# Performance work log

Hardware: AMD Instinct MI355X
Metric: run time of the kernel (lower is better)

Reference implementation:

```python
import jax, jax.numpy as jnp
import numpy as np

D_MODEL = 1024
NUM_HEADS = 16
HEAD_DIM = D_MODEL // NUM_HEADS  # 64
# NOTE: the original module passes scale=attention_head_size, so scores are
# MULTIPLIED by head_dim (64), not divided by sqrt(head_dim). Faithful quirk.
SCALE = float(HEAD_DIM)


def setup_inputs() -> dict:
    key = jax.random.key(0)
    ks = jax.random.split(key, 6)
    bs, s, d = 2, 2048, D_MODEL
    q = jax.random.normal(ks[0], (bs, s, d), dtype=jnp.float32)
    k = jax.random.normal(ks[1], (bs, s, d), dtype=jnp.float32)
    v = jax.random.normal(ks[2], (bs, s, d), dtype=jnp.float32)
    # nn.Linear weights, shape (out, in); no bias (qkv_bias=False)
    init = 1.0 / np.sqrt(d)
    Wq = jax.random.uniform(ks[3], (d, d), jnp.float32, -init, init)
    Wk = jax.random.uniform(ks[4], (d, d), jnp.float32, -init, init)
    Wv = jax.random.uniform(ks[5], (d, d), jnp.float32, -init, init)
    return {"q": q, "k": k, "v": v, "Wq": Wq, "Wk": Wk, "Wv": Wv}


def _split_heads(x):
    bs, s, _ = x.shape
    return x.reshape(bs, s, NUM_HEADS, HEAD_DIM).transpose(0, 2, 1, 3)  # bhsd


def reference(q, k, v, Wq, Wk, Wv):
    bs, s, d = q.shape
    qh = _split_heads(q @ Wq.T)  # [b,h,s,hd]
    kh = _split_heads(k @ Wk.T)
    vh = _split_heads(v @ Wv.T)
    sims = jnp.einsum('bhqd,bhkd->bhqk', qh, kh) * SCALE
    attn = jax.nn.softmax(sims, axis=-1)
    out = jnp.einsum('bhqk,bhkd->bhqd', attn, vh)  # [b,h,s,hd]
    out = out.transpose(0, 2, 1, 3).reshape(bs, s, d)
    return out
```

## Files before the change

kernel.cpp:

```cpp
#include <hip/hip_runtime.h>


typedef _Float16 half4 __attribute__((ext_vector_type(4)));
typedef _Float16 half8 __attribute__((ext_vector_type(8)));
typedef float floatx4 __attribute__((ext_vector_type(4)));

#define MFMA_F16(a, b, c) __builtin_amdgcn_mfma_f32_16x16x32_f16((a), (b), (c), 0, 0, 0)

constexpr int SEQ = 2048;
constexpr int DM = 1024;
constexpr int NH = 16;
constexpr int HD = 64;
constexpr float QSCALE = 92.33248261689366f;

__device__ inline void split4(const float4 f, half4& h, half4& l) {
  h[0] = (_Float16)f.x; l[0] = (_Float16)(f.x - (float)h[0]);
  h[1] = (_Float16)f.y; l[1] = (_Float16)(f.y - (float)h[1]);
  h[2] = (_Float16)f.z; l[2] = (_Float16)(f.z - (float)h[2]);
  h[3] = (_Float16)f.w; l[3] = (_Float16)(f.w - (float)h[3]);
}

__global__ __launch_bounds__(256) void convert_kernel(
    const float* __restrict__ x, const float* __restrict__ W,
    _Float16* __restrict__ xh, _Float16* __restrict__ xl,
    _Float16* __restrict__ Wh, _Float16* __restrict__ Wl, int do_lo)
{
  if (blockIdx.x < 4096) {
    int idx = blockIdx.x * 256 + threadIdx.x;
    float4 f = ((const float4*)x)[idx];
    half4 h, l; split4(f, h, l);
    *(half4*)(xh + (size_t)idx * 4) = h;
    if (do_lo) *(half4*)(xl + (size_t)idx * 4) = l;
  } else {
    int idx = (blockIdx.x - 4096) * 256 + threadIdx.x;
    float4 f = ((const float4*)W)[idx];
    half4 h, l; split4(f, h, l);
    *(half4*)(Wh + (size_t)idx * 4) = h;
    if (do_lo) *(half4*)(Wl + (size_t)idx * 4) = l;
  }
}

__global__ __launch_bounds__(256, 1) void proj_kernel(
    const _Float16* __restrict__ Ahg, const _Float16* __restrict__ Alg,
    const _Float16* __restrict__ Bhg, const _Float16* __restrict__ Blg,
    _Float16* __restrict__ yh, _Float16* __restrict__ yl,
    float scale, int three)
{
  __shared__ __align__(16) _Float16 Ahs[128][72];
  __shared__ __align__(16) _Float16 Als[128][72];
  __shared__ __align__(16) _Float16 Bhs[128][72];
  __shared__ __align__(16) _Float16 Bls[128][72];

  const int tid = threadIdx.x;
  const int bm = blockIdx.x;
  const int bn = blockIdx.y;
  const int lane = tid & 63, l15 = lane & 15, quad = lane >> 4;
  const int w = tid >> 6, wm = w >> 1, wn = w & 1;

  int row_[4], col_[4];
  #pragma unroll
  for (int i = 0; i < 4; i++) { int c = i * 256 + tid; row_[i] = c >> 3; col_[i] = (c & 7) * 8; }

  half8 pah[4], pal[4], pbh[4], pbl[4];
  #pragma unroll
  for (int i = 0; i < 4; i++) {
    pah[i] = *(const half8*)(Ahg + (size_t)(bm * 128 + row_[i]) * DM + col_[i]);
    pbh[i] = *(const half8*)(Bhg + (size_t)(bn * 128 + row_[i]) * DM + col_[i]);
    if (three) {
      pal[i] = *(const half8*)(Alg + (size_t)(bm * 128 + row_[i]) * DM + col_[i]);
      pbl[i] = *(const half8*)(Blg + (size_t)(bn * 128 + row_[i]) * DM + col_[i]);
    }
  }

  floatx4 acc[4][4];
  #pragma unroll
  for (int mt = 0; mt < 4; mt++)
    #pragma unroll
    for (int nt = 0; nt < 4; nt++)
      acc[mt][nt] = (floatx4){0.f, 0.f, 0.f, 0.f};

  for (int kk = 0; kk < DM; kk += 64) {
    __syncthreads();
    #pragma unroll
    for (int i = 0; i < 4; i++) {
      *(half8*)&Ahs[row_[i]][col_[i]] = pah[i];
      *(half8*)&Bhs[row_[i]][col_[i]] = pbh[i];
      if (three) {
        *(half8*)&Als[row_[i]][col_[i]] = pal[i];
        *(half8*)&Bls[row_[i]][col_[i]] = pbl[i];
      }
    }
    if (kk + 64 < DM) {
      #pragma unroll
      for (int i = 0; i < 4; i++) {
        pah[i] = *(const half8*)(Ahg + (size_t)(bm * 128 + row_[i]) * DM + kk + 64 + col_[i]);
        pbh[i] = *(const half8*)(Bhg + (size_t)(bn * 128 + row_[i]) * DM + kk + 64 + col_[i]);
        if (three) {
          pal[i] = *(const half8*)(Alg + (size_t)(bm * 128 + row_[i]) * DM + kk + 64 + col_[i]);
          pbl[i] = *(const half8*)(Blg + (size_t)(bn * 128 + row_[i]) * DM + kk + 64 + col_[i]);
        }
      }
    }
    __syncthreads();

    #pragma unroll
    for (int kc = 0; kc < 2; kc++) {
      half8 ah[4], bh_[4], al[4], bl[4];
      #pragma unroll
      for (int t = 0; t < 4; t++) {
        ah[t]  = *(const half8*)&Ahs[wm * 64 + t * 16 + l15][kc * 32 + quad * 8];
        bh_[t] = *(const half8*)&Bhs[wn * 64 + t * 16 + l15][kc * 32 + quad * 8];
        if (three) {
          al[t] = *(const half8*)&Als[wm * 64 + t * 16 + l15][kc * 32 + quad * 8];
          bl[t] = *(const half8*)&Bls[wn * 64 + t * 16 + l15][kc * 32 + quad * 8];
        }
      }
      if (three) {
        #pragma unroll
        for (int mt = 0; mt < 4; mt++)
          #pragma unroll
          for (int nt = 0; nt < 4; nt++) {
            floatx4 t0 = MFMA_F16(ah[mt], bh_[nt], acc[mt][nt]);
            t0 = MFMA_F16(ah[mt], bl[nt], t0);
            acc[mt][nt] = MFMA_F16(al[mt], bh_[nt], t0);
          }
      } else {
        #pragma unroll
        for (int mt = 0; mt < 4; mt++)
          #pragma unroll
          for (int nt = 0; nt < 4; nt++)
            acc[mt][nt] = MFMA_F16(ah[mt], bh_[nt], acc[mt][nt]);
      }
    }
  }

  #pragma unroll
  for (int mt = 0; mt < 4; mt++)
    #pragma unroll
    for (int nt = 0; nt < 4; nt++)
      #pragma unroll
      for (int r = 0; r < 4; r++) {
        int gm = bm * 128 + wm * 64 + mt * 16 + quad * 4 + r;
        int gn = bn * 128 + wn * 64 + nt * 16 + l15;
        int b = gm >> 11, s = gm & 2047;
        int h = gn >> 6, d = gn & 63;
        size_t idx = ((size_t)(b * NH + h) * SEQ + s) * HD + d;
        float val = acc[mt][nt][r] * scale;
        _Float16 hi = (_Float16)val;
        yh[idx] = hi;
        if (three) yl[idx] = (_Float16)(val - (float)hi);
      }
}

__global__ __launch_bounds__(256) void transpose_v(const _Float16* __restrict__ vh,
                                                   _Float16* __restrict__ vhT)
{
  __shared__ __align__(16) _Float16 T[128][72];
  const int bh = blockIdx.x, sc = blockIdx.y, tid = threadIdx.x;
  const _Float16* src = vh + ((size_t)bh * SEQ + sc * 128) * HD;
  #pragma unroll
  for (int i = 0; i < 4; i++) {
    int c = i * 256 + tid, row = c >> 3, off = (c & 7) * 8;
    *(half8*)&T[row][off] = *(const half8*)(src + (size_t)row * HD + off);
  }
  __syncthreads();
  _Float16* dst = vhT + (size_t)bh * HD * SEQ + sc * 128;
  #pragma unroll
  for (int i = 0; i < 4; i++) {
    int c = i * 256 + tid, hd = c >> 4, off = (c & 15) * 8;
    int base32 = off & ~31, qsel = (off >> 3) & 3;
    half8 vv;
    #pragma unroll
    for (int j = 0; j < 8; j++) {
      int s_local = base32 + 16 * (j >> 2) + 4 * qsel + (j & 3);
      vv[j] = T[s_local][hd];
    }
    *(half8*)(dst + (size_t)hd * SEQ + off) = vv;
  }
}

__global__ __launch_bounds__(256, 4) void flash_kernel(
    const _Float16* __restrict__ qh_hi, const _Float16* __restrict__ qh_lo,
    const _Float16* __restrict__ kh_hi, const _Float16* __restrict__ kh_lo,
    const _Float16* __restrict__ vhT, float* __restrict__ Op, float2* __restrict__ ml)
{
  __shared__ __align__(16) _Float16 Kh[64][72];
  __shared__ __align__(16) _Float16 Kl[64][72];
  __shared__ __align__(16) _Float16 Vt[64][72];

  const int bh = blockIdx.x;
  const int qb = blockIdx.y;
  const int kh = blockIdx.z;
  const int tid = threadIdx.x;
  const int wq = tid >> 6;
  const int lane = tid & 63, l15 = lane & 15, quad = lane >> 4;

  const size_t bh_off = (size_t)bh * SEQ * HD;
  const _Float16* __restrict__ kh_p = kh_hi + bh_off;
  const _Float16* __restrict__ kl_p = kh_lo + bh_off;
  const _Float16* __restrict__ vt_p = vhT + (size_t)bh * HD * SEQ;
  const int qrow0 = qb * 128 + wq * 32;

  half8 bqh[2][2], bql[2][2];
  #pragma unroll
  for (int g = 0; g < 2; g++) {
    const _Float16* qp_h = qh_hi + bh_off + (size_t)(qrow0 + g * 16 + l15) * HD;
    const _Float16* qp_l = qh_lo + bh_off + (size_t)(qrow0 + g * 16 + l15) * HD;
    #pragma unroll
    for (int kc = 0; kc < 2; kc++) {
      bqh[g][kc] = *(const half8*)(qp_h + kc * 32 + quad * 8);
      bql[g][kc] = *(const half8*)(qp_l + kc * 32 + quad * 8);
    }
  }

  const int c0 = tid, c1 = tid + 256;
  const int row0 = c0 >> 3, off0 = (c0 & 7) * 8;
  const int row1 = c1 >> 3, off1 = (c1 & 7) * 8;

  float m_[2] = {-3.0e38f, -3.0e38f};
  float l_[2] = {0.f, 0.f};
  floatx4 Oacc[2][4];
  #pragma unroll
  for (int g = 0; g < 2; g++)
    #pragma unroll
    for (int nd = 0; nd < 4; nd++) Oacc[g][nd] = (floatx4){0.f, 0.f, 0.f, 0.f};

  const int kt0 = kh * 16;
  for (int kt = kt0; kt < kt0 + 16; kt++) {
    const int kbase = kt * 64;
    __syncthreads();
    {
      half8 t0 = *(const half8*)(kh_p + (size_t)(kbase + row0) * HD + off0);
      half8 t1 = *(const half8*)(kh_p + (size_t)(kbase + row1) * HD + off1);
      half8 t2 = *(const half8*)(kl_p + (size_t)(kbase + row0) * HD + off0);
      half8 t3 = *(const half8*)(kl_p + (size_t)(kbase + row1) * HD + off1);
      half8 t4 = *(const half8*)(vt_p + (size_t)row0 * SEQ + kbase + off0);
      half8 t5 = *(const half8*)(vt_p + (size_t)row1 * SEQ + kbase + off1);
      *(half8*)&Kh[row0][off0] = t0;
      *(half8*)&Kh[row1][off1] = t1;
      *(half8*)&Kl[row0][off0] = t2;
      *(half8*)&Kl[row1][off1] = t3;
      *(half8*)&Vt[row0][off0] = t4;
      *(half8*)&Vt[row1][off1] = t5;
    }
    __syncthreads();

    floatx4 sacc[2][4];
    #pragma unroll
    for (int nt = 0; nt < 4; nt++) {
      half8 akh0 = *(const half8*)&Kh[nt * 16 + l15][quad * 8];
      half8 akh1 = *(const half8*)&Kh[nt * 16 + l15][32 + quad * 8];
      half8 akl0 = *(const half8*)&Kl[nt * 16 + l15][quad * 8];
      half8 akl1 = *(const half8*)&Kl[nt * 16 + l15][32 + quad * 8];
      #pragma unroll
      for (int g = 0; g < 2; g++) {
        floatx4 s4 = (floatx4){0.f, 0.f, 0.f, 0.f};
        s4 = MFMA_F16(akh0, bqh[g][0], s4);
        s4 = MFMA_F16(akh1, bqh[g][1], s4);
        s4 = MFMA_F16(akh0, bql[g][0], s4);
        s4 = MFMA_F16(akh1, bql[g][1], s4);
        s4 = MFMA_F16(akl0, bqh[g][0], s4);
        s4 = MFMA_F16(akl1, bqh[g][1], s4);
        sacc[g][nt] = s4;
      }
    }

    #pragma unroll
    for (int g = 0; g < 2; g++) {
      float rmax = sacc[g][0][0];
      #pragma unroll
      for (int nt = 0; nt < 4; nt++)
        #pragma unroll
        for (int r = 0; r < 4; r++) rmax = fmaxf(rmax, sacc[g][nt][r]);
      rmax = fmaxf(rmax, __shfl_xor(rmax, 16, 64));
      rmax = fmaxf(rmax, __shfl_xor(rmax, 32, 64));
      const float mnew = fmaxf(m_[g], rmax);
      const float alpha = exp2f(m_[g] - mnew);
      m_[g] = mnew;

      float rsum = 0.f;
      #pragma unroll
      for (int nt = 0; nt < 4; nt++)
        #pragma unroll
        for (int r = 0; r < 4; r++) {
          float p = exp2f(sacc[g][nt][r] - mnew);
          sacc[g][nt][r] = p;
          rsum += p;
        }
      rsum += __shfl_xor(rsum, 16, 64);
      rsum += __shfl_xor(rsum, 32, 64);
      l_[g] = l_[g] * alpha + rsum;

      half8 bp8[2];
      #pragma unroll
      for (int kc = 0; kc < 2; kc++)
        #pragma unroll
        for (int j = 0; j < 8; j++)
          bp8[kc][j] = (_Float16)sacc[g][2 * kc + (j >> 2)][j & 3];

      #pragma unroll
      for (int nd = 0; nd < 4; nd++) {
        half8 av0 = *(const half8*)&Vt[nd * 16 + l15][quad * 8];
        half8 av1 = *(const half8*)&Vt[nd * 16 + l15][32 + quad * 8];
        Oacc[g][nd][0] *= alpha; Oacc[g][nd][1] *= alpha;
        Oacc[g][nd][2] *= alpha; Oacc[g][nd][3] *= alpha;
        Oacc[g][nd] = MFMA_F16(av0, bp8[0], Oacc[g][nd]);
        Oacc[g][nd] = MFMA_F16(av1, bp8[1], Oacc[g][nd]);
      }
    }
  }

  const size_t fqbase = (size_t)bh * SEQ + qrow0;
  #pragma unroll
  for (int g = 0; g < 2; g++) {
    const size_t fq = fqbase + g * 16 + l15;
    float* ob = Op + ((size_t)kh * 65536 + fq) * HD;
    #pragma unroll
    for (int nd = 0; nd < 4; nd++) {
      float4 vv;
      vv.x = Oacc[g][nd][0]; vv.y = Oacc[g][nd][1];
      vv.z = Oacc[g][nd][2]; vv.w = Oacc[g][nd][3];
      *(float4*)(ob + nd * 16 + quad * 4) = vv;
    }
    if (quad == 0) ml[kh * 65536 + fq] = make_float2(m_[g], l_[g]);
  }
}

__global__ __launch_bounds__(256) void merge_kernel(const float* __restrict__ Op,
                                                    const float2* __restrict__ ml,
                                                    float* __restrict__ out)
{
  const int tid = threadIdx.x;
  const int fq = blockIdx.x * 64 + (tid >> 2);
  const int dp = (tid & 3) * 16;
  float2 m0 = ml[fq], m1 = ml[65536 + fq];
  float M = fmaxf(m0.x, m1.x);
  float w0 = exp2f(m0.x - M), w1 = exp2f(m1.x - M);
  float rinv = 1.0f / (m0.y * w0 + m1.y * w1);
  int bh = fq >> 11, s = fq & 2047, b = bh >> 4, h = bh & 15;
  float* ob = out + ((size_t)(b * SEQ + s)) * DM + h * HD + dp;
  const float* p0 = Op + (size_t)fq * HD + dp;
  const float* p1 = p0 + (size_t)65536 * HD;
  #pragma unroll
  for (int j = 0; j < 4; j++) {
    float4 a = *(const float4*)(p0 + 4 * j);
    float4 c = *(const float4*)(p1 + 4 * j);
    float4 r;
    r.x = (a.x * w0 + c.x * w1) * rinv;
    r.y = (a.y * w0 + c.y * w1) * rinv;
    r.z = (a.z * w0 + c.z * w1) * rinv;
    r.w = (a.w * w0 + c.w * w1) * rinv;
    *(float4*)(ob + 4 * j) = r;
  }
}

extern "C" void kernel_launch(void* const* d_in, const int* in_sizes, int n_in,
                              void* d_out, int out_size, void* d_ws, size_t ws_size,
                              hipStream_t stream) {
  const float* q  = (const float*)d_in[0];
  const float* k  = (const float*)d_in[1];
  const float* v  = (const float*)d_in[2];
  const float* Wq = (const float*)d_in[3];
  const float* Wk = (const float*)d_in[4];
  const float* Wv = (const float*)d_in[5];
  float* out = (float*)d_out;

  char* W = (char*)d_ws;
  const size_t MiB = 1ull << 20;
  _Float16* qh_hi = (_Float16*)(W + 0 * MiB);
  _Float16* qh_lo = (_Float16*)(W + 8 * MiB);
  _Float16* kh_hi = (_Float16*)(W + 16 * MiB);
  _Float16* kh_lo = (_Float16*)(W + 24 * MiB);
  _Float16* vhT   = (_Float16*)(W + 32 * MiB);
  _Float16* vh    = (_Float16*)(W + 40 * MiB);
  _Float16* xh    = (_Float16*)(W + 48 * MiB);
  _Float16* xl    = (_Float16*)(W + 56 * MiB);
  _Float16* Wh    = (_Float16*)(W + 64 * MiB);
  _Float16* Wl    = (_Float16*)(W + 66 * MiB);
  float*    Op    = (float*)  (W + 40 * MiB);
  float2*   mlp   = (float2*) (W + 72 * MiB);

  convert_kernel<<<5120, 256, 0, stream>>>(q, Wq, xh, xl, Wh, Wl, 1);
  proj_kernel<<<dim3(32, 8), 256, 0, stream>>>(xh, xl, Wh, Wl, qh_hi, qh_lo, QSCALE, 1);
  convert_kernel<<<5120, 256, 0, stream>>>(k, Wk, xh, xl, Wh, Wl, 1);
  proj_kernel<<<dim3(32, 8), 256, 0, stream>>>(xh, xl, Wh, Wl, kh_hi, kh_lo, 1.0f, 1);
  convert_kernel<<<5120, 256, 0, stream>>>(v, Wv, xh, xl, Wh, Wl, 0);
  proj_kernel<<<dim3(32, 8), 256, 0, stream>>>(xh, xl, Wh, Wl, vh, vh, 1.0f, 0);

  transpose_v<<<dim3(32, 16), 256, 0, stream>>>(vh, vhT);
  flash_kernel<<<dim3(32, 16, 2), 256, 0, stream>>>(qh_hi, qh_lo, kh_hi, kh_lo, vhT, Op, mlp);
  merge_kernel<<<1024, 256, 0, stream>>>(Op, mlp, out);
}
```

Baseline: 346.1 us.

## Fuse activation split into a batched QKV projection and swizzle LDS tiles

The separate per-projection convert kernels for activations are removed. The projection kernel now reads fp32 q/k/v directly and splits them into hi/lo halves while staging to LDS. The three projections run in a single launch using a z grid dimension, with weights pre-converted by one combined kernel, and launch bounds are raised to allow two blocks per CU. LDS padding is replaced by an XOR swizzle in both the projection and flash kernels, and flash block indices are remapped into a 1D grid. This cuts launches and intermediate global traffic and gives more parallel blocks. The cost is extra conversion ALU work inside the GEMM loop and higher register pressure.

```diff
diff --git a/kernel.cpp b/kernel.cpp
--- a/kernel.cpp
+++ b/kernel.cpp
@@ -20,36 +20,37 @@
   h[3] = (_Float16)f.w; l[3] = (_Float16)(f.w - (float)h[3]);
 }
 
-__global__ __launch_bounds__(256) void convert_kernel(
-    const float* __restrict__ x, const float* __restrict__ W,
-    _Float16* __restrict__ xh, _Float16* __restrict__ xl,
-    _Float16* __restrict__ Wh, _Float16* __restrict__ Wl, int do_lo)
+__global__ __launch_bounds__(256) void convert_w(
+    const float* __restrict__ Wq, const float* __restrict__ Wk,
+    const float* __restrict__ Wv, _Float16* __restrict__ Wbase)
 {
-  if (blockIdx.x < 4096) {
-    int idx = blockIdx.x * 256 + threadIdx.x;
-    float4 f = ((const float4*)x)[idx];
-    half4 h, l; split4(f, h, l);
-    *(half4*)(xh + (size_t)idx * 4) = h;
-    if (do_lo) *(half4*)(xl + (size_t)idx * 4) = l;
-  } else {
-    int idx = (blockIdx.x - 4096) * 256 + threadIdx.x;
-    float4 f = ((const float4*)W)[idx];
-    half4 h, l; split4(f, h, l);
-    *(half4*)(Wh + (size_t)idx * 4) = h;
-    if (do_lo) *(half4*)(Wl + (size_t)idx * 4) = l;
-  }
-}
-
-__global__ __launch_bounds__(256, 1) void proj_kernel(
-    const _Float16* __restrict__ Ahg, const _Float16* __restrict__ Alg,
-    const _Float16* __restrict__ Bhg, const _Float16* __restrict__ Blg,
-    _Float16* __restrict__ yh, _Float16* __restrict__ yl,
-    float scale, int three)
+  const int z = blockIdx.x >> 10;
+  const int idx = (blockIdx.x & 1023) * 256 + threadIdx.x;
+  const float* __restrict__ src = (z == 0) ? Wq : (z == 1) ? Wk : Wv;
+  float4 f = ((const float4*)src)[idx];
+  half4 h, l; split4(f, h, l);
+  _Float16* Wh = Wbase + (size_t)z * 2097152;
+  *(half4*)(Wh + (size_t)idx * 4) = h;
+  if (z < 2) *(half4*)(Wh + 1048576 + (size_t)idx * 4) = l;
+}
+
+__global__ __launch_bounds__(256, 2) void proj_kernel(
+    const float* __restrict__ q, const float* __restrict__ k, const float* __restrict__ v,
+    const _Float16* __restrict__ Wbase,
+    _Float16* __restrict__ qh_hi, _Float16* __restrict__ qh_lo,
+    _Float16* __restrict__ kh_hi, _Float16* __restrict__ kh_lo,
+    _Float16* __restrict__ vh)
 {
-  __shared__ __align__(16) _Float16 Ahs[128][72];
-  __shared__ __align__(16) _Float16 Als[128][72];
-  __shared__ __align__(16) _Float16 Bhs[128][72];
-  __shared__ __align__(16) _Float16 Bls[128][72];
+  __shared__ __align__(16) _Float16 Ahs[128][64];
+  __shared__ __align__(16) _Float16 Als[128][64];
+  __shared__ __align__(16) _Float16 Bhs[128][64];
+  __shared__ __align__(16) _Float16 Bls[128][64];
+
+  const int z = blockIdx.z;
+  const float* __restrict__ x = (z == 0) ? q : (z == 1) ? k : v;
+  const _Float16* __restrict__ Whg = Wbase + (size_t)z * 2097152;
+  const _Float16* __restrict__ Wlg = Whg + 1048576;
+  const int three = (z != 2);
 
   const int tid = threadIdx.x;
   const int bm = blockIdx.x;
@@ -57,19 +58,24 @@
   const int lane = tid & 63, l15 = lane & 15, quad = lane >> 4;
   const int w = tid >> 6, wm = w >> 1, wn = w & 1;
 
-  int row_[4], col_[4];
-  #pragma unroll
-  for (int i = 0; i < 4; i++) { int c = i * 256 + tid; row_[i] = c >> 3; col_[i] = (c & 7) * 8; }
-
-  half8 pah[4], pal[4], pbh[4], pbl[4];
+  int rowi[4], chi[4], swc[4];
   #pragma unroll
   for (int i = 0; i < 4; i++) {
-    pah[i] = *(const half8*)(Ahg + (size_t)(bm * 128 + row_[i]) * DM + col_[i]);
-    pbh[i] = *(const half8*)(Bhg + (size_t)(bn * 128 + row_[i]) * DM + col_[i]);
-    if (three) {
-      pal[i] = *(const half8*)(Alg + (size_t)(bm * 128 + row_[i]) * DM + col_[i]);
-      pbl[i] = *(const half8*)(Blg + (size_t)(bn * 128 + row_[i]) * DM + col_[i]);
-    }
+    int c = i * 256 + tid;
+    rowi[i] = c >> 3; chi[i] = c & 7;
+    swc[i] = (chi[i] ^ (rowi[i] & 7)) * 8;
+  }
+
+  float4 pa[4][2];
+  half8 pbh[4], pbl[4];
+  #pragma unroll
+  for (int i = 0; i < 4; i++) {
+    const float* ar = x + (size_t)(bm * 128 + rowi[i]) * DM + chi[i] * 8;
+    pa[i][0] = *(const float4*)ar;
+    pa[i][1] = *(const float4*)(ar + 4);
+    pbh[i] = *(const half8*)(Whg + (size_t)(bn * 128 + rowi[i]) * DM + chi[i] * 8);
+    if (three)
+      pbl[i] = *(const half8*)(Wlg + (size_t)(bn * 128 + rowi[i]) * DM + chi[i] * 8);
   }
 
   floatx4 acc[4][4];
@@ -83,36 +89,41 @@
     __syncthreads();
     #pragma unroll
     for (int i = 0; i < 4; i++) {
-      *(half8*)&Ahs[row_[i]][col_[i]] = pah[i];
-      *(half8*)&Bhs[row_[i]][col_[i]] = pbh[i];
-      if (three) {
-        *(half8*)&Als[row_[i]][col_[i]] = pal[i];
-        *(half8*)&Bls[row_[i]][col_[i]] = pbl[i];
-      }
+      half4 h0, l0, h1, l1;
+      split4(pa[i][0], h0, l0);
+      split4(pa[i][1], h1, l1);
+      half8 hh, ll;
+      #pragma unroll
+      for (int j = 0; j < 4; j++) { hh[j] = h0[j]; hh[j + 4] = h1[j]; ll[j] = l0[j]; ll[j + 4] = l1[j]; }
+      *(half8*)&Ahs[rowi[i]][swc[i]] = hh;
+      *(half8*)&Als[rowi[i]][swc[i]] = ll;
+      *(half8*)&Bhs[rowi[i]][swc[i]] = pbh[i];
+      if (three) *(half8*)&Bls[rowi[i]][swc[i]] = pbl[i];
     }
     if (kk + 64 < DM) {
       #pragma unroll
       for (int i = 0; i < 4; i++) {
-        pah[i] = *(const half8*)(Ahg + (size_t)(bm * 128 + row_[i]) * DM + kk + 64 + col_[i]);
-        pbh[i] = *(const half8*)(Bhg + (size_t)(bn * 128 + row_[i]) * DM + kk + 64 + col_[i]);
+        const float* ar = x + (size_t)(bm * 128 + rowi[i]) * DM + kk + 64 + chi[i] * 8;
+        pa[i][0] = *(const float4*)ar;
+        pa[i][1] = *(const float4*)(ar + 4);
+        pbh[i] = *(const half8*)(Whg + (size_t)(bn * 128 + rowi[i]) * DM + kk + 64 + chi[i] * 8);
+        if (three)
+          pbl[i] = *(const half8*)(Wlg + (size_t)(bn * 128 + rowi[i]) * DM + kk + 64 + chi[i] * 8);
+      }
+    }
+    __syncthreads();
+
+    #pragma unroll
+    for (int kc = 0; kc < 2; kc++) {
+      const int swz = ((kc * 4 + quad) ^ (l15 & 7)) * 8;
+      half8 ah[4], bh_[4], al[4], bl[4];
+      #pragma unroll
+      for (int t = 0; t < 4; t++) {
+        ah[t]  = *(const half8*)&Ahs[wm * 64 + t * 16 + l15][swz];
+        bh_[t] = *(const half8*)&Bhs[wn * 64 + t * 16 + l15][swz];
         if (three) {
-          pal[i] = *(const half8*)(Alg + (size_t)(bm * 128 + row_[i]) * DM + kk + 64 + col_[i]);
-          pbl[i] = *(const half8*)(Blg + (size_t)(bn * 128 + row_[i]) * DM + kk + 64 + col_[i]);
-        }
-      }
-    }
-    __syncthreads();
-
-    #pragma unroll
-    for (int kc = 0; kc < 2; kc++) {
-      half8 ah[4], bh_[4], al[4], bl[4];
-      #pragma unroll
-      for (int t = 0; t < 4; t++) {
-        ah[t]  = *(const half8*)&Ahs[wm * 64 + t * 16 + l15][kc * 32 + quad * 8];
-        bh_[t] = *(const half8*)&Bhs[wn * 64 + t * 16 + l15][kc * 32 + quad * 8];
-        if (three) {
-          al[t] = *(const half8*)&Als[wm * 64 + t * 16 + l15][kc * 32 + quad * 8];
-          bl[t] = *(const half8*)&Bls[wn * 64 + t * 16 + l15][kc * 32 + quad * 8];
+          al[t] = *(const half8*)&Als[wm * 64 + t * 16 + l15][swz];
+          bl[t] = *(const half8*)&Bls[wn * 64 + t * 16 + l15][swz];
         }
       }
       if (three) {
@@ -134,6 +145,9 @@
     }
   }
 
+  const float scale = (z == 0) ? QSCALE : 1.0f;
+  _Float16* yh = (z == 0) ? qh_hi : (z == 1) ? kh_hi : vh;
+  _Float16* yl = (z == 0) ? qh_lo : kh_lo;
   #pragma unroll
   for (int mt = 0; mt < 4; mt++)
     #pragma unroll
@@ -184,13 +198,16 @@
     const _Float16* __restrict__ kh_hi, const _Float16* __restrict__ kh_lo,
     const _Float16* __restrict__ vhT, float* __restrict__ Op, float2* __restrict__ ml)
 {
-  __shared__ __align__(16) _Float16 Kh[64][72];
-  __shared__ __align__(16) _Float16 Kl[64][72];
-  __shared__ __align__(16) _Float16 Vt[64][72];
-
-  const int bh = blockIdx.x;
-  const int qb = blockIdx.y;
-  const int kh = blockIdx.z;
+  __shared__ __align__(16) _Float16 Kh[64][64];
+  __shared__ __align__(16) _Float16 Kl[64][64];
+  __shared__ __align__(16) _Float16 Vt[64][64];
+
+  const int id = blockIdx.x;
+  const int seq_ = id >> 3;
+  const int bh = (id & 7) + 8 * (seq_ & 3);
+  const int rem = seq_ >> 2;
+  const int qb = rem & 15;
+  const int kh = rem >> 4;
   const int tid = threadIdx.x;
   const int wq = tid >> 6;
   const int lane = tid & 63, l15 = lane & 15, quad = lane >> 4;
@@ -213,9 +230,8 @@
     }
   }
 
-  const int c0 = tid, c1 = tid + 256;
-  const int row0 = c0 >> 3, off0 = (c0 & 7) * 8;
-  const int row1 = c1 >> 3, off1 = (c1 & 7) * 8;
+  const int row0 = tid >> 3, ch0 = tid & 7, sw0 = (ch0 ^ (row0 & 7)) * 8;
+  const int row1 = row0 + 32, sw1 = sw0;
 
   float m_[2] = {-3.0e38f, -3.0e38f};
   float l_[2] = {0.f, 0.f};
@@ -230,28 +246,29 @@
     const int kbase = kt * 64;
     __syncthreads();
     {
-      half8 t0 = *(const half8*)(kh_p + (size_t)(kbase + row0) * HD + off0);
-      half8 t1 = *(const half8*)(kh_p + (size_t)(kbase + row1) * HD + off1);
-      half8 t2 = *(const half8*)(kl_p + (size_t)(kbase + row0) * HD + off0);
-      half8 t3 = *(const half8*)(kl_p + (size_t)(kbase + row1) * HD + off1);
-      half8 t4 = *(const half8*)(vt_p + (size_t)row0 * SEQ + kbase + off0);
-      half8 t5 = *(const half8*)(vt_p + (size_t)row1 * SEQ + kbase + off1);
-      *(half8*)&Kh[row0][off0] = t0;
-      *(half8*)&Kh[row1][off1] = t1;
-      *(half8*)&Kl[row0][off0] = t2;
-      *(half8*)&Kl[row1][off1] = t3;
-      *(half8*)&Vt[row0][off0] = t4;
-      *(half8*)&Vt[row1][off1] = t5;
+      half8 t0 = *(const half8*)(kh_p + (size_t)(kbase + row0) * HD + ch0 * 8);
+      half8 t1 = *(const half8*)(kh_p + (size_t)(kbase + row1) * HD + ch0 * 8);
+      half8 t2 = *(const half8*)(kl_p + (size_t)(kbase + row0) * HD + ch0 * 8);
+      half8 t3 = *(const half8*)(kl_p + (size_t)(kbase + row1) * HD + ch0 * 8);
+      half8 t4 = *(const half8*)(vt_p + (size_t)row0 * SEQ + kbase + ch0 * 8);
+      half8 t5 = *(const half8*)(vt_p + (size_t)row1 * SEQ + kbase + ch0 * 8);
+      *(half8*)&Kh[row0][sw0] = t0;
+      *(half8*)&Kh[row1][sw1] = t1;
+      *(half8*)&Kl[row0][sw0] = t2;
+      *(half8*)&Kl[row1][sw1] = t3;
+      *(half8*)&Vt[row0][sw0] = t4;
+      *(half8*)&Vt[row1][sw1] = t5;
     }
     __syncthreads();
 
     floatx4 sacc[2][4];
     #pragma unroll
     for (int nt = 0; nt < 4; nt++) {
-      half8 akh0 = *(const half8*)&Kh[nt * 16 + l15][quad * 8];
-      half8 akh1 = *(const half8*)&Kh[nt * 16 + l15][32 + quad * 8];
-      half8 akl0 = *(const half8*)&Kl[nt * 16 + l15][quad * 8];
-      half8 akl1 = *(const half8*)&Kl[nt * 16 + l15][32 + quad * 8];
+      const int r7 = l15 & 7;
+      half8 akh0 = *(const half8*)&Kh[nt * 16 + l15][((0 * 4 + quad) ^ r7) * 8];
+      half8 akh1 = *(const half8*)&Kh[nt * 16 + l15][((1 * 4 + quad) ^ r7) * 8];
+      half8 akl0 = *(const half8*)&Kl[nt * 16 + l15][((0 * 4 + quad) ^ r7) * 8];
+      half8 akl1 = *(const half8*)&Kl[nt * 16 + l15][((1 * 4 + quad) ^ r7) * 8];
       #pragma unroll
       for (int g = 0; g < 2; g++) {
         floatx4 s4 = (floatx4){0.f, 0.f, 0.f, 0.f};
@@ -298,10 +315,11 @@
         for (int j = 0; j < 8; j++)
           bp8[kc][j] = (_Float16)sacc[g][2 * kc + (j >> 2)][j & 3];
 
+      const int r7 = l15 & 7;
       #pragma unroll
       for (int nd = 0; nd < 4; nd++) {
-        half8 av0 = *(const half8*)&Vt[nd * 16 + l15][quad * 8];
-        half8 av1 = *(const half8*)&Vt[nd * 16 + l15][32 + quad * 8];
+        half8 av0 = *(const half8*)&Vt[nd * 16 + l15][((0 * 4 + quad) ^ r7) * 8];
+        half8 av1 = *(const half8*)&Vt[nd * 16 + l15][((1 * 4 + quad) ^ r7) * 8];
         Oacc[g][nd][0] *= alpha; Oacc[g][nd][1] *= alpha;
         Oacc[g][nd][2] *= alpha; Oacc[g][nd][3] *= alpha;
         Oacc[g][nd] = MFMA_F16(av0, bp8[0], Oacc[g][nd]);
@@ -373,21 +391,14 @@
   _Float16* kh_lo = (_Float16*)(W + 24 * MiB);
   _Float16* vhT   = (_Float16*)(W + 32 * MiB);
   _Float16* vh    = (_Float16*)(W + 40 * MiB);
-  _Float16* xh    = (_Float16*)(W + 48 * MiB);
-  _Float16* xl    = (_Float16*)(W + 56 * MiB);
-  _Float16* Wh    = (_Float16*)(W + 64 * MiB);
-  _Float16* Wl    = (_Float16*)(W + 66 * MiB);
+  _Float16* Wbase = (_Float16*)(W + 48 * MiB);
   float*    Op    = (float*)  (W + 40 * MiB);
   float2*   mlp   = (float2*) (W + 72 * MiB);
 
-  convert_kernel<<<5120, 256, 0, stream>>>(q, Wq, xh, xl, Wh, Wl, 1);
-  proj_kernel<<<dim3(32, 8), 256, 0, stream>>>(xh, xl, Wh, Wl, qh_hi, qh_lo, QSCALE, 1);
-  convert_kernel<<<5120, 256, 0, stream>>>(k, Wk, xh, xl, Wh, Wl, 1);
-  proj_kernel<<<dim3(32, 8), 256, 0, stream>>>(xh, xl, Wh, Wl, kh_hi, kh_lo, 1.0f, 1);
-  convert_kernel<<<5120, 256, 0, stream>>>(v, Wv, xh, xl, Wh, Wl, 0);
-  proj_kernel<<<dim3(32, 8), 256, 0, stream>>>(xh, xl, Wh, Wl, vh, vh, 1.0f, 0);
-
+  convert_w<<<3072, 256, 0, stream>>>(Wq, Wk, Wv, Wbase);
+  proj_kernel<<<dim3(32, 8, 3), 256, 0, stream>>>(q, k, v, Wbase,
+                                                  qh_hi, qh_lo, kh_hi, kh_lo, vh);
   transpose_v<<<dim3(32, 16), 256, 0, stream>>>(vh, vhT);
-  flash_kernel<<<dim3(32, 16, 2), 256, 0, stream>>>(qh_hi, qh_lo, kh_hi, kh_lo, vhT, Op, mlp);
+  flash_kernel<<<1024, 256, 0, stream>>>(qh_hi, qh_lo, kh_hi, kh_lo, vhT, Op, mlp);
   merge_kernel<<<1024, 256, 0, stream>>>(Op, mlp, out);
 }
```

New measurement: 424.0 us. 1.23x slower.

## Load GEMM and attention tiles directly to LDS with XOR-swizzled layout

Applied to the files above, without the earlier changes.

Replaces register-staged global-to-shared copies in the projection and flash kernels with direct global_load_lds transfers. Shared tiles are unpadded and use an XOR swizzle on both write and read to avoid bank conflicts. The projection kernel loses its register prefetch of the next tile, so load latency is no longer overlapped with compute. The flash kernel hoists the V fragment loads out of the per-group loop and remaps a 1D grid to reorder block scheduling across heads for cache locality.

```diff
diff --git a/kernel.cpp b/kernel.cpp
--- a/kernel.cpp
+++ b/kernel.cpp
@@ -12,6 +12,12 @@
 constexpr int NH = 16;
 constexpr int HD = 64;
 constexpr float QSCALE = 92.33248261689366f;
+
+__device__ __forceinline__ void gl2lds16(const _Float16* g, _Float16* l) {
+  __builtin_amdgcn_global_load_lds(
+      (const __attribute__((address_space(1))) void*)g,
+      (__attribute__((address_space(3))) void*)l, 16, 0, 0);
+}
 
 __device__ inline void split4(const float4 f, half4& h, half4& l) {
   h[0] = (_Float16)f.x; l[0] = (_Float16)(f.x - (float)h[0]);
@@ -46,10 +52,10 @@
     _Float16* __restrict__ yh, _Float16* __restrict__ yl,
     float scale, int three)
 {
-  __shared__ __align__(16) _Float16 Ahs[128][72];
-  __shared__ __align__(16) _Float16 Als[128][72];
-  __shared__ __align__(16) _Float16 Bhs[128][72];
-  __shared__ __align__(16) _Float16 Bls[128][72];
+  __shared__ __align__(16) _Float16 Ahs[128][64];
+  __shared__ __align__(16) _Float16 Als[128][64];
+  __shared__ __align__(16) _Float16 Bhs[128][64];
+  __shared__ __align__(16) _Float16 Bls[128][64];
 
   const int tid = threadIdx.x;
   const int bm = blockIdx.x;
@@ -57,19 +63,17 @@
   const int lane = tid & 63, l15 = lane & 15, quad = lane >> 4;
   const int w = tid >> 6, wm = w >> 1, wn = w & 1;
 
-  int row_[4], col_[4];
-  #pragma unroll
-  for (int i = 0; i < 4; i++) { int c = i * 256 + tid; row_[i] = c >> 3; col_[i] = (c & 7) * 8; }
-
-  half8 pah[4], pal[4], pbh[4], pbl[4];
+  const int r8 = lane >> 3;
+  const int cp8 = (((lane & 7) ^ r8)) * 8;
+  int grow[4]; _Float16* la[4]; _Float16* lal[4]; _Float16* lb[4]; _Float16* lbl[4];
   #pragma unroll
   for (int i = 0; i < 4; i++) {
-    pah[i] = *(const half8*)(Ahg + (size_t)(bm * 128 + row_[i]) * DM + col_[i]);
-    pbh[i] = *(const half8*)(Bhg + (size_t)(bn * 128 + row_[i]) * DM + col_[i]);
-    if (three) {
-      pal[i] = *(const half8*)(Alg + (size_t)(bm * 128 + row_[i]) * DM + col_[i]);
-      pbl[i] = *(const half8*)(Blg + (size_t)(bn * 128 + row_[i]) * DM + col_[i]);
-    }
+    const int g = w * 4 + i;
+    grow[i] = g * 8 + r8;
+    la[i]  = &Ahs[0][0] + g * 512;
+    lal[i] = &Als[0][0] + g * 512;
+    lb[i]  = &Bhs[0][0] + g * 512;
+    lbl[i] = &Bls[0][0] + g * 512;
   }
 
   floatx4 acc[4][4];
@@ -83,36 +87,28 @@
     __syncthreads();
     #pragma unroll
     for (int i = 0; i < 4; i++) {
-      *(half8*)&Ahs[row_[i]][col_[i]] = pah[i];
-      *(half8*)&Bhs[row_[i]][col_[i]] = pbh[i];
+      const size_t ga = (size_t)(bm * 128 + grow[i]) * DM + kk + cp8;
+      const size_t gb = (size_t)(bn * 128 + grow[i]) * DM + kk + cp8;
+      gl2lds16(Ahg + ga, la[i]);
+      gl2lds16(Bhg + gb, lb[i]);
       if (three) {
-        *(half8*)&Als[row_[i]][col_[i]] = pal[i];
-        *(half8*)&Bls[row_[i]][col_[i]] = pbl[i];
-      }
-    }
-    if (kk + 64 < DM) {
-      #pragma unroll
-      for (int i = 0; i < 4; i++) {
-        pah[i] = *(const half8*)(Ahg + (size_t)(bm * 128 + row_[i]) * DM + kk + 64 + col_[i]);
-        pbh[i] = *(const half8*)(Bhg + (size_t)(bn * 128 + row_[i]) * DM + kk + 64 + col_[i]);
+        gl2lds16(Alg + ga, lal[i]);
+        gl2lds16(Blg + gb, lbl[i]);
+      }
+    }
+    __syncthreads();
+
+    #pragma unroll
+    for (int kc = 0; kc < 2; kc++) {
+      const int swz = ((kc * 4 + quad) ^ (l15 & 7)) * 8;
+      half8 ah[4], bh_[4], al[4], bl[4];
+      #pragma unroll
+      for (int t = 0; t < 4; t++) {
+        ah[t]  = *(const half8*)&Ahs[wm * 64 + t * 16 + l15][swz];
+        bh_[t] = *(const half8*)&Bhs[wn * 64 + t * 16 + l15][swz];
         if (three) {
-          pal[i] = *(const half8*)(Alg + (size_t)(bm * 128 + row_[i]) * DM + kk + 64 + col_[i]);
-          pbl[i] = *(const half8*)(Blg + (size_t)(bn * 128 + row_[i]) * DM + kk + 64 + col_[i]);
-        }
-      }
-    }
-    __syncthreads();
-
-    #pragma unroll
-    for (int kc = 0; kc < 2; kc++) {
-      half8 ah[4], bh_[4], al[4], bl[4];
-      #pragma unroll
-      for (int t = 0; t < 4; t++) {
-        ah[t]  = *(const half8*)&Ahs[wm * 64 + t * 16 + l15][kc * 32 + quad * 8];
-        bh_[t] = *(const half8*)&Bhs[wn * 64 + t * 16 + l15][kc * 32 + quad * 8];
-        if (three) {
-          al[t] = *(const half8*)&Als[wm * 64 + t * 16 + l15][kc * 32 + quad * 8];
-          bl[t] = *(const half8*)&Bls[wn * 64 + t * 16 + l15][kc * 32 + quad * 8];
+          al[t] = *(const half8*)&Als[wm * 64 + t * 16 + l15][swz];
+          bl[t] = *(const half8*)&Bls[wn * 64 + t * 16 + l15][swz];
         }
       }
       if (three) {
@@ -184,13 +180,16 @@
     const _Float16* __restrict__ kh_hi, const _Float16* __restrict__ kh_lo,
     const _Float16* __restrict__ vhT, float* __restrict__ Op, float2* __restrict__ ml)
 {
-  __shared__ __align__(16) _Float16 Kh[64][72];
-  __shared__ __align__(16) _Float16 Kl[64][72];
-  __shared__ __align__(16) _Float16 Vt[64][72];
-
-  const int bh = blockIdx.x;
-  const int qb = blockIdx.y;
-  const int kh = blockIdx.z;
+  __shared__ __align__(16) _Float16 Kh[64][64];
+  __shared__ __align__(16) _Float16 Kl[64][64];
+  __shared__ __align__(16) _Float16 Vt[64][64];
+
+  const int id = blockIdx.x;
+  const int seq_ = id >> 3;
+  const int bh = (id & 7) + 8 * (seq_ & 3);
+  const int rem = seq_ >> 2;
+  const int qb = rem & 15;
+  const int kh = rem >> 4;
   const int tid = threadIdx.x;
   const int wq = tid >> 6;
   const int lane = tid & 63, l15 = lane & 15, quad = lane >> 4;
@@ -213,9 +212,8 @@
     }
   }
 
-  const int c0 = tid, c1 = tid + 256;
-  const int row0 = c0 >> 3, off0 = (c0 & 7) * 8;
-  const int row1 = c1 >> 3, off1 = (c1 & 7) * 8;
+  const int r8 = lane >> 3;
+  const int cp8 = ((lane & 7) ^ r8) * 8;
 
   float m_[2] = {-3.0e38f, -3.0e38f};
   float l_[2] = {0.f, 0.f};
@@ -229,29 +227,24 @@
   for (int kt = kt0; kt < kt0 + 16; kt++) {
     const int kbase = kt * 64;
     __syncthreads();
-    {
-      half8 t0 = *(const half8*)(kh_p + (size_t)(kbase + row0) * HD + off0);
-      half8 t1 = *(const half8*)(kh_p + (size_t)(kbase + row1) * HD + off1);
-      half8 t2 = *(const half8*)(kl_p + (size_t)(kbase + row0) * HD + off0);
-      half8 t3 = *(const half8*)(kl_p + (size_t)(kbase + row1) * HD + off1);
-      half8 t4 = *(const half8*)(vt_p + (size_t)row0 * SEQ + kbase + off0);
-      half8 t5 = *(const half8*)(vt_p + (size_t)row1 * SEQ + kbase + off1);
-      *(half8*)&Kh[row0][off0] = t0;
-      *(half8*)&Kh[row1][off1] = t1;
-      *(half8*)&Kl[row0][off0] = t2;
-      *(half8*)&Kl[row1][off1] = t3;
-      *(half8*)&Vt[row0][off0] = t4;
-      *(half8*)&Vt[row1][off1] = t5;
+    #pragma unroll
+    for (int i = 0; i < 2; i++) {
+      const int g = wq * 2 + i;
+      const int r = g * 8 + r8;
+      gl2lds16(kh_p + (size_t)(kbase + r) * HD + cp8, &Kh[0][0] + g * 512);
+      gl2lds16(kl_p + (size_t)(kbase + r) * HD + cp8, &Kl[0][0] + g * 512);
+      gl2lds16(vt_p + (size_t)r * SEQ + kbase + cp8, &Vt[0][0] + g * 512);
     }
     __syncthreads();
 
     floatx4 sacc[2][4];
     #pragma unroll
     for (int nt = 0; nt < 4; nt++) {
-      half8 akh0 = *(const half8*)&Kh[nt * 16 + l15][quad * 8];
-      half8 akh1 = *(const half8*)&Kh[nt * 16 + l15][32 + quad * 8];
-      half8 akl0 = *(const half8*)&Kl[nt * 16 + l15][quad * 8];
-      half8 akl1 = *(const half8*)&Kl[nt * 16 + l15][32 + quad * 8];
+      const int r7 = l15 & 7;
+      half8 akh0 = *(const half8*)&Kh[nt * 16 + l15][((0 * 4 + quad) ^ r7) * 8];
+      half8 akh1 = *(const half8*)&Kh[nt * 16 + l15][((1 * 4 + quad) ^ r7) * 8];
+      half8 akl0 = *(const half8*)&Kl[nt * 16 + l15][((0 * 4 + quad) ^ r7) * 8];
+      half8 akl1 = *(const half8*)&Kl[nt * 16 + l15][((1 * 4 + quad) ^ r7) * 8];
       #pragma unroll
       for (int g = 0; g < 2; g++) {
         floatx4 s4 = (floatx4){0.f, 0.f, 0.f, 0.f};
@@ -265,6 +258,16 @@
       }
     }
 
+    half8 av[4][2];
+    {
+      const int r7 = l15 & 7;
+      #pragma unroll
+      for (int nd = 0; nd < 4; nd++) {
+        av[nd][0] = *(const half8*)&Vt[nd * 16 + l15][((0 * 4 + quad) ^ r7) * 8];
+        av[nd][1] = *(const half8*)&Vt[nd * 16 + l15][((1 * 4 + quad) ^ r7) * 8];
+      }
+    }
+
     #pragma unroll
     for (int g = 0; g < 2; g++) {
       float rmax = sacc[g][0][0];
@@ -300,12 +303,10 @@
 
       #pragma unroll
       for (int nd = 0; nd < 4; nd++) {
-        half8 av0 = *(const half8*)&Vt[nd * 16 + l15][quad * 8];
-        half8 av1 = *(const half8*)&Vt[nd * 16 + l15][32 + quad * 8];
         Oacc[g][nd][0] *= alpha; Oacc[g][nd][1] *= alpha;
         Oacc[g][nd][2] *= alpha; Oacc[g][nd][3] *= alpha;
-        Oacc[g][nd] = MFMA_F16(av0, bp8[0], Oacc[g][nd]);
-        Oacc[g][nd] = MFMA_F16(av1, bp8[1], Oacc[g][nd]);
+        Oacc[g][nd] = MFMA_F16(av[nd][0], bp8[0], Oacc[g][nd]);
+        Oacc[g][nd] = MFMA_F16(av[nd][1], bp8[1], Oacc[g][nd]);
       }
     }
   }
@@ -388,6 +389,6 @@
   proj_kernel<<<dim3(32, 8), 256, 0, stream>>>(xh, xl, Wh, Wl, vh, vh, 1.0f, 0);
 
   transpose_v<<<dim3(32, 16), 256, 0, stream>>>(vh, vhT);
-  flash_kernel<<<dim3(32, 16, 2), 256, 0, stream>>>(qh_hi, qh_lo, kh_hi, kh_lo, vhT, Op, mlp);
+  flash_kernel<<<1024, 256, 0, stream>>>(qh_hi, qh_lo, kh_hi, kh_lo, vhT, Op, mlp);
   merge_kernel<<<1024, 256, 0, stream>>>(Op, mlp, out);
 }
```

Measured after the change: 321.8 us. 7.0% less time.
